# Kernel tuning notes

Hardware: AMD Instinct MI355X
Metric: run time of the kernel (lower is better)

The kernel has to match this reference:

```python
import jax, jax.numpy as jnp
import numpy as np

N = 50000       # num_nodes
R = 8           # num_relations
H = 64          # hidden_channels
C = 16          # num_classes
E = 1_600_000   # num edges (avg degree 32)
T = 8192        # number of 'author' target nodes (first T nodes after to_homogeneous)


def setup_inputs() -> dict:
    key = jax.random.key(0)
    ks = jax.random.split(key, 12)
    s = 0.02
    return {
        "edge_index": jax.random.randint(ks[0], (2, E), 0, N),
        "edge_type": jax.random.randint(ks[1], (E,), 0, R),
        "num_target": T,
        # conv1 (featureless: weight is an embedding table [R, N, H], root is [N, H])
        "weight1": jax.random.normal(ks[2], (R, N, H), jnp.float32) * s,
        "root1": jax.random.normal(ks[3], (N, H), jnp.float32) * s,
        "bias1": jnp.zeros((H,), jnp.float32),
        # conv2
        "weight2": jax.random.normal(ks[4], (R, H, H), jnp.float32) * s,
        "root2": jax.random.normal(ks[5], (H, H), jnp.float32) * s,
        "bias2": jnp.zeros((H,), jnp.float32),
        # linear head
        "lin_w": jax.random.normal(ks[6], (H, C), jnp.float32) * s,
        "lin_b": jnp.zeros((C,), jnp.float32),
    }


def reference(edge_index, edge_type, num_target, weight1, root1, bias1,
              weight2, root2, bias2, lin_w, lin_b):
    src, dst = edge_index[0], edge_index[1]
    E_ = src.shape[0]

    # PyG RGCNConv aggregates with MEAN per relation, then sums over relations.
    # Count edges per (dst node, relation) to form the per-relation mean denominator.
    seg = dst * R + edge_type                          # [E] combined (node, relation) id
    cnt = jax.ops.segment_sum(jnp.ones((E_,), jnp.float32), seg, num_segments=N * R)
    scale = (1.0 / jnp.maximum(cnt, 1.0))[seg]         # [E]

    # ---- conv1: x is None -> message = weight1[edge_type][src] (embedding lookup) ----
    m1 = weight1[edge_type, src] * scale[:, None]      # [E, H]
    h1 = jax.ops.segment_sum(m1, dst, num_segments=N)  # [N, H]
    h1 = h1 + root1 + bias1                            # root1[arange(N)] == root1
    h1 = jax.nn.elu(h1)

    # ---- conv2: message = h1[src] @ weight2[edge_type] ----
    # Precompute per-relation node transforms [R, N, H], then gather per edge.
    hr = jnp.einsum('nh,rhk->rnk', h1, weight2)        # [R, N, H]
    m2 = hr[edge_type, src] * scale[:, None]           # [E, H]
    h2 = jax.ops.segment_sum(m2, dst, num_segments=N)  # [N, H]
    h2 = h2 + h1 @ root2 + bias2
    h2 = jax.nn.elu(h2)

    # ---- linear head on the target ('author') node slice ----
    out = h2[:num_target] @ lin_w + lin_b              # [T, C]
    return out
```

## Files before the change

### kernel.cpp

```cpp
#include <hip/hip_runtime.h>

#define NNODES 50000
#define NREL   8
#define HID    64
#define NCLS   16
#define NEDGE  1600000
#define NTGT   8192
#define NBINS  (NNODES * NREL)
#define CHUNK  1024
#define NCHUNK ((NBINS + CHUNK - 1) / CHUNK)
#define C1PART 12500

__device__ __forceinline__ float elu1(float x) { return x > 0.f ? x : expm1f(x); }

__device__ __forceinline__ int pack_rec(int src, int rel, int cnt) {
  return src | (rel << 16) | (cnt << 19);
}

__global__ void count_kernel(const int* __restrict__ ei, const int* __restrict__ et,
                             int* __restrict__ cnt, int* __restrict__ epos) {
  int e4 = (blockIdx.x * blockDim.x + threadIdx.x) * 4;
  if (e4 >= NEDGE) return;
  int4 d = *(const int4*)(ei + NEDGE + e4);
  int4 r = *(const int4*)(et + e4);
  int4 p;
  p.x = atomicAdd(&cnt[d.x * NREL + r.x], 1);
  p.y = atomicAdd(&cnt[d.y * NREL + r.y], 1);
  p.z = atomicAdd(&cnt[d.z * NREL + r.z], 1);
  p.w = atomicAdd(&cnt[d.w * NREL + r.w], 1);
  *(int4*)(epos + e4) = p;
}

__global__ void chunk_sum_kernel(const int* __restrict__ cnt, int* __restrict__ csum) {
  __shared__ int sw[4];
  int t = threadIdx.x, lane = t & 63, wid = t >> 6;
  int i = blockIdx.x * CHUNK + t * 4;
  int s = 0;
  if (i < NBINS) { int4 c = *(const int4*)(cnt + i); s = c.x + c.y + c.z + c.w; }
#pragma unroll
  for (int off = 32; off >= 1; off >>= 1) s += __shfl_xor(s, off);
  if (lane == 0) sw[wid] = s;
  __syncthreads();
  if (t == 0) csum[blockIdx.x] = sw[0] + sw[1] + sw[2] + sw[3];
}

__global__ void scan_csum_kernel(const int* __restrict__ csum, int* __restrict__ cbase) {
  __shared__ int sw[8];
  int t = threadIdx.x, lane = t & 63, wid = t >> 6;
  int v0 = (t < NCHUNK) ? csum[t] : 0;
  int v = v0;
#pragma unroll
  for (int off = 1; off < 64; off <<= 1) {
    int u = __shfl_up(v, off);
    if (lane >= off) v += u;
  }
  if (lane == 63) sw[wid] = v;
  __syncthreads();
  if (t == 0) {
    int run = 0;
#pragma unroll
    for (int j = 0; j < 8; ++j) { int x = sw[j]; sw[j] = run; run += x; }
  }
  __syncthreads();
  if (t < NCHUNK) cbase[t] = sw[wid] + (v - v0);
}

__global__ void scan_write_kernel(const int* __restrict__ cnt, const int* __restrict__ cbase,
                                  int* __restrict__ binptr) {
  __shared__ int sw[4];
  int t = threadIdx.x, lane = t & 63, wid = t >> 6;
  int i = blockIdx.x * CHUNK + t * 4;
  int4 c = make_int4(0, 0, 0, 0);
  if (i < NBINS) c = *(const int4*)(cnt + i);
  int p0 = c.x, p1 = p0 + c.y, p2 = p1 + c.z, s = p2 + c.w;
  int v = s;
#pragma unroll
  for (int off = 1; off < 64; off <<= 1) {
    int u = __shfl_up(v, off);
    if (lane >= off) v += u;
  }
  if (lane == 63) sw[wid] = v;
  __syncthreads();
  if (t == 0) {
    int run = 0;
#pragma unroll
    for (int j = 0; j < 4; ++j) { int x = sw[j]; sw[j] = run; run += x; }
  }
  __syncthreads();
  if (i < NBINS) {
    int excl = cbase[blockIdx.x] + sw[wid] + (v - s);
    *(int4*)(binptr + i) = make_int4(excl, excl + p0, excl + p1, excl + p2);
  }
  if (blockIdx.x == 0 && t == 0) binptr[NBINS] = NEDGE;
}

__global__ void scatter_kernel(const int* __restrict__ ei, const int* __restrict__ et,
                               const int* __restrict__ epos, const int* __restrict__ binptr,
                               int* __restrict__ epo) {
  int e4 = (blockIdx.x * blockDim.x + threadIdx.x) * 4;
  if (e4 >= NEDGE) return;
  int4 sv = *(const int4*)(ei + e4);
  int4 dv = *(const int4*)(ei + NEDGE + e4);
  int4 rv = *(const int4*)(et + e4);
  int4 pv = *(const int4*)(epos + e4);
  int srcs[4] = {sv.x, sv.y, sv.z, sv.w};
  int dsts[4] = {dv.x, dv.y, dv.z, dv.w};
  int rels[4] = {rv.x, rv.y, rv.z, rv.w};
  int poss[4] = {pv.x, pv.y, pv.z, pv.w};
#pragma unroll
  for (int j = 0; j < 4; ++j) {
    int bin = dsts[j] * NREL + rels[j];
    int b = binptr[bin];
    int c = binptr[bin + 1] - b;
    epo[b + poss[j]] = pack_rec(srcs[j], rels[j], c);
  }
}

__global__ __launch_bounds__(256) void conv1_kernel(
    const int* __restrict__ binptr, const int* __restrict__ epo,
    const float* __restrict__ w1, const float* __restrict__ root1,
    const float* __restrict__ bias1, float* __restrict__ h1, int nodeOff) {
  int wave = nodeOff + blockIdx.x * 4 + (threadIdx.x >> 6);
  if (wave >= NNODES) return;
  int lane = threadIdx.x & 63;
  int g = lane >> 4;
  int col = (lane & 15) << 2;
  int b0 = binptr[wave * NREL], b8 = binptr[wave * NREL + NREL];
  float4 acc = make_float4(0.f, 0.f, 0.f, 0.f);
  for (int eb = b0; eb < b8; eb += 64) {
    int mb = min(64, b8 - eb);
    int q = epo[eb + min(lane, mb - 1)];
    for (int j = 0; j < mb; j += 32) {
      float4 a[8]; float sc[8];
#pragma unroll
      for (int u = 0; u < 8; ++u) {
        int e0 = j + u * 4;
        if (e0 < mb) {
          int ei = e0 + g;
          int eic = min(ei, mb - 1);
          int rec = __shfl(q, eic);
          int src = rec & 0xFFFF;
          int rel = (rec >> 16) & 7;
          int cnt = ((unsigned)rec) >> 19;
          float s = 1.0f / (float)cnt;
          sc[u] = (ei < mb) ? s : 0.f;
          a[u] = *(const float4*)(w1 + (((size_t)(unsigned)(rel * NNODES + src)) << 6) + col);
        } else {
          sc[u] = 0.f;
          a[u] = make_float4(0.f, 0.f, 0.f, 0.f);
        }
      }
#pragma unroll
      for (int u = 0; u < 8; ++u) {
        acc.x = fmaf(a[u].x, sc[u], acc.x);
        acc.y = fmaf(a[u].y, sc[u], acc.y);
        acc.z = fmaf(a[u].z, sc[u], acc.z);
        acc.w = fmaf(a[u].w, sc[u], acc.w);
      }
    }
  }
#pragma unroll
  for (int off = 16; off < 64; off <<= 1) {
    acc.x += __shfl_xor(acc.x, off);
    acc.y += __shfl_xor(acc.y, off);
    acc.z += __shfl_xor(acc.z, off);
    acc.w += __shfl_xor(acc.w, off);
  }
  if (g == 0) {
    const float* rp = root1 + (((size_t)wave) << 6) + col;
    float4 r = *(const float4*)rp;
    float4 bz = *(const float4*)(bias1 + col);
    float4 v;
    v.x = elu1(acc.x + r.x + bz.x);
    v.y = elu1(acc.y + r.y + bz.y);
    v.z = elu1(acc.z + r.z + bz.z);
    v.w = elu1(acc.w + r.w + bz.w);
    *(float4*)(h1 + (((size_t)wave) << 6) + col) = v;
  }
}

__global__ __launch_bounds__(256) void conv2a_kernel(
    const int* __restrict__ binptr, const int* __restrict__ epo,
    const float* __restrict__ h1, float* __restrict__ agg, int nodeBase, int nloc) {
  int wv = blockIdx.x * 4 + (threadIdx.x >> 6);
  if (wv >= nloc * NREL) return;
  int lane = threadIdx.x & 63;
  int g = lane >> 4;
  int col = (lane & 15) << 2;
  int r = wv & 7;
  int bin = (nodeBase + (wv >> 3)) * NREL + r;
  int bb = binptr[bin], ee = binptr[bin + 1];
  float4 s = make_float4(0.f, 0.f, 0.f, 0.f);
  for (int e = bb; e < ee; e += 64) {
    int mb = min(64, ee - e);
    int q = epo[e + min(lane, mb - 1)];
    for (int j = 0; j < mb; j += 16) {
      float4 a[4]; float vld[4];
#pragma unroll
      for (int u = 0; u < 4; ++u) {
        int e0 = j + u * 4;
        if (e0 < mb) {
          int ei = e0 + g;
          int eic = min(ei, mb - 1);
          int src = __shfl(q, eic) & 0xFFFF;
          vld[u] = (ei < mb) ? 1.f : 0.f;
          a[u] = *(const float4*)(h1 + (((size_t)(unsigned)src) << 6) + col);
        } else {
          vld[u] = 0.f;
          a[u] = make_float4(0.f, 0.f, 0.f, 0.f);
        }
      }
#pragma unroll
      for (int u = 0; u < 4; ++u) {
        s.x = fmaf(a[u].x, vld[u], s.x);
        s.y = fmaf(a[u].y, vld[u], s.y);
        s.z = fmaf(a[u].z, vld[u], s.z);
        s.w = fmaf(a[u].w, vld[u], s.w);
      }
    }
  }
#pragma unroll
  for (int off = 16; off < 64; off <<= 1) {
    s.x += __shfl_xor(s.x, off);
    s.y += __shfl_xor(s.y, off);
    s.z += __shfl_xor(s.z, off);
    s.w += __shfl_xor(s.w, off);
  }
  if (g == 0) {
    float scl = (ee > bb) ? 1.0f / (float)(ee - bb) : 0.f;
    float4 o = make_float4(s.x * scl, s.y * scl, s.z * scl, s.w * scl);
    *(float4*)(agg + (((size_t)wv) << 6) + col) = o;
  }
}

__global__ __launch_bounds__(256, 4) void conv2b_kernel(
    const float* __restrict__ agg, const float* __restrict__ h1,
    const float* __restrict__ w2, const float* __restrict__ root2,
    const float* __restrict__ bias2, const float* __restrict__ lin_w,
    const float* __restrict__ lin_b, float* __restrict__ out, int nodeBase) {
  __shared__ float sW[HID * HID];
  int t = threadIdx.x, lane = t & 63, wid = t >> 6;
  int ln0 = blockIdx.x * 8 + wid * 2;
  float bz = bias2[lane];
  float o0 = bz, o1 = bz;
  for (int r = 0; r < NREL; ++r) {
    if (r) __syncthreads();
#pragma unroll
    for (int i = 0; i < 4; ++i)
      *(float4*)(sW + t * 4 + i * 1024) = *(const float4*)(w2 + (r << 12) + t * 4 + i * 1024);
    __syncthreads();
    const float* a0 = agg + (((size_t)((ln0 + 0) * NREL + r)) << 6);
    const float* a1 = agg + (((size_t)((ln0 + 1) * NREL + r)) << 6);
#pragma unroll 16
    for (int k = 0; k < HID; ++k) {
      float w = sW[(k << 6) + lane];
      o0 = fmaf(a0[k], w, o0);
      o1 = fmaf(a1[k], w, o1);
    }
  }
  __syncthreads();
#pragma unroll
  for (int i = 0; i < 4; ++i)
    *(float4*)(sW + t * 4 + i * 1024) = *(const float4*)(root2 + t * 4 + i * 1024);
  __syncthreads();
  int g0 = nodeBase + ln0;
  const float* r0p = h1 + ((size_t)(g0 + 0) << 6);
  const float* r1p = h1 + ((size_t)(g0 + 1) << 6);
#pragma unroll 16
  for (int k = 0; k < HID; ++k) {
    float w = sW[(k << 6) + lane];
    o0 = fmaf(r0p[k], w, o0);
    o1 = fmaf(r1p[k], w, o1);
  }
  __syncthreads();
  int row0 = wid * 2;
  sW[row0 * 65 + lane] = elu1(o0);
  sW[(row0 + 1) * 65 + lane] = elu1(o1);
  float* lw = sW + 8 * 65;
  *(float4*)(lw + t * 4) = *(const float4*)(lin_w + t * 4);
  __syncthreads();
  if (t < 8 * NCLS) {
    int n = t >> 4, c = t & 15;
    float accv = lin_b[c];
#pragma unroll 16
    for (int l = 0; l < HID; ++l)
      accv = fmaf(sW[n * 65 + l], lw[l * NCLS + c], accv);
    out[((size_t)(nodeBase + blockIdx.x * 8 + n)) * NCLS + c] = accv;
  }
}

extern "C" void kernel_launch(void* const* d_in, const int* in_sizes, int n_in,
                              void* d_out, int out_size, void* d_ws, size_t ws_size,
                              hipStream_t stream) {
  const int*   ei    = (const int*)d_in[0];
  const int*   et    = (const int*)d_in[1];
  const float* w1    = (const float*)d_in[3];
  const float* root1 = (const float*)d_in[4];
  const float* bias1 = (const float*)d_in[5];
  const float* w2    = (const float*)d_in[6];
  const float* root2 = (const float*)d_in[7];
  const float* bias2 = (const float*)d_in[8];
  const float* lin_w = (const float*)d_in[9];
  const float* lin_b = (const float*)d_in[10];
  float* out = (float*)d_out;

  char* ws = (char*)d_ws;
  float* h1     = (float*)ws;
  int*   cnt    = (int*)ws;
  int*   epos   = (int*)(ws + (size_t)NBINS * 4);
  char*  p      = ws + (size_t)NNODES * HID * 4;
  int*   binptr = (int*)p;  p += ((size_t)(NBINS + 1) * 4 + 255) & ~(size_t)255;
  int*   csum   = (int*)p;  p += ((size_t)NCHUNK * 4 + 255) & ~(size_t)255;
  int*   cbase  = (int*)p;  p += ((size_t)NCHUNK * 4 + 255) & ~(size_t)255;
  int*   epo    = (int*)p;  p += (size_t)NEDGE * 4;
  float* agg    = (float*)p;
  size_t fixed  = (size_t)(p - ws);
  int chunk = (fixed + (size_t)NTGT * NREL * HID * 4 <= ws_size) ? NTGT : NTGT / 2;

  hipMemsetAsync(cnt, 0, (size_t)NBINS * sizeof(int), stream);
  count_kernel<<<(NEDGE / 4 + 255) / 256, 256, 0, stream>>>(ei, et, cnt, epos);
  chunk_sum_kernel<<<NCHUNK, 256, 0, stream>>>(cnt, csum);
  scan_csum_kernel<<<1, 512, 0, stream>>>(csum, cbase);
  scan_write_kernel<<<NCHUNK, 256, 0, stream>>>(cnt, cbase, binptr);
  scatter_kernel<<<(NEDGE / 4 + 255) / 256, 256, 0, stream>>>(ei, et, epos, binptr, epo);
  for (int s4 = 0; s4 < 4; ++s4)
    conv1_kernel<<<C1PART / 4, 256, 0, stream>>>(binptr, epo, w1, root1, bias1, h1,
                                                 s4 * C1PART);
  for (int c = 0; c < NTGT / chunk; ++c) {
    conv2a_kernel<<<(chunk * NREL) / 4, 256, 0, stream>>>(binptr, epo, h1, agg, c * chunk, chunk);
    conv2b_kernel<<<chunk / 8, 256, 0, stream>>>(agg, h1, w2, root2, bias2, lin_w, lin_b,
                                                 out, c * chunk);
  }
}
```

Before: 420.4 us.

## Pad per-bin counters to 64-byte stride and launch conv1 as one kernel

```diff
diff --git a/kernel.cpp b/kernel.cpp
--- a/kernel.cpp
+++ b/kernel.cpp
@@ -9,7 +9,6 @@
 #define NBINS  (NNODES * NREL)
 #define CHUNK  1024
 #define NCHUNK ((NBINS + CHUNK - 1) / CHUNK)
-#define C1PART 12500
 
 __device__ __forceinline__ float elu1(float x) { return x > 0.f ? x : expm1f(x); }
 
@@ -24,10 +23,10 @@
   int4 d = *(const int4*)(ei + NEDGE + e4);
   int4 r = *(const int4*)(et + e4);
   int4 p;
-  p.x = atomicAdd(&cnt[d.x * NREL + r.x], 1);
-  p.y = atomicAdd(&cnt[d.y * NREL + r.y], 1);
-  p.z = atomicAdd(&cnt[d.z * NREL + r.z], 1);
-  p.w = atomicAdd(&cnt[d.w * NREL + r.w], 1);
+  p.x = atomicAdd(&cnt[(d.x * NREL + r.x) << 4], 1);
+  p.y = atomicAdd(&cnt[(d.y * NREL + r.y) << 4], 1);
+  p.z = atomicAdd(&cnt[(d.z * NREL + r.z) << 4], 1);
+  p.w = atomicAdd(&cnt[(d.w * NREL + r.w) << 4], 1);
   *(int4*)(epos + e4) = p;
 }
 
@@ -36,7 +35,9 @@
   int t = threadIdx.x, lane = t & 63, wid = t >> 6;
   int i = blockIdx.x * CHUNK + t * 4;
   int s = 0;
-  if (i < NBINS) { int4 c = *(const int4*)(cnt + i); s = c.x + c.y + c.z + c.w; }
+  if (i < NBINS)
+    s = cnt[(size_t)(i + 0) << 4] + cnt[(size_t)(i + 1) << 4] +
+        cnt[(size_t)(i + 2) << 4] + cnt[(size_t)(i + 3) << 4];
 #pragma unroll
   for (int off = 32; off >= 1; off >>= 1) s += __shfl_xor(s, off);
   if (lane == 0) sw[wid] = s;
@@ -70,9 +71,14 @@
   __shared__ int sw[4];
   int t = threadIdx.x, lane = t & 63, wid = t >> 6;
   int i = blockIdx.x * CHUNK + t * 4;
-  int4 c = make_int4(0, 0, 0, 0);
-  if (i < NBINS) c = *(const int4*)(cnt + i);
-  int p0 = c.x, p1 = p0 + c.y, p2 = p1 + c.z, s = p2 + c.w;
+  int c0 = 0, c1 = 0, c2 = 0, c3 = 0;
+  if (i < NBINS) {
+    c0 = cnt[(size_t)(i + 0) << 4];
+    c1 = cnt[(size_t)(i + 1) << 4];
+    c2 = cnt[(size_t)(i + 2) << 4];
+    c3 = cnt[(size_t)(i + 3) << 4];
+  }
+  int p0 = c0, p1 = p0 + c1, p2 = p1 + c2, s = p2 + c3;
   int v = s;
 #pragma unroll
   for (int off = 1; off < 64; off <<= 1) {
@@ -119,8 +125,8 @@
 __global__ __launch_bounds__(256) void conv1_kernel(
     const int* __restrict__ binptr, const int* __restrict__ epo,
     const float* __restrict__ w1, const float* __restrict__ root1,
-    const float* __restrict__ bias1, float* __restrict__ h1, int nodeOff) {
-  int wave = nodeOff + blockIdx.x * 4 + (threadIdx.x >> 6);
+    const float* __restrict__ bias1, float* __restrict__ h1) {
+  int wave = blockIdx.x * 4 + (threadIdx.x >> 6);
   if (wave >= NNODES) return;
   int lane = threadIdx.x & 63;
   int g = lane >> 4;
@@ -305,27 +311,28 @@
   float* out = (float*)d_out;
 
   char* ws = (char*)d_ws;
-  float* h1     = (float*)ws;
-  int*   cnt    = (int*)ws;
-  int*   epos   = (int*)(ws + (size_t)NBINS * 4);
-  char*  p      = ws + (size_t)NNODES * HID * 4;
+  int*   epos   = (int*)ws;
+  char*  p      = ws + (size_t)NEDGE * 4;
   int*   binptr = (int*)p;  p += ((size_t)(NBINS + 1) * 4 + 255) & ~(size_t)255;
   int*   csum   = (int*)p;  p += ((size_t)NCHUNK * 4 + 255) & ~(size_t)255;
   int*   cbase  = (int*)p;  p += ((size_t)NCHUNK * 4 + 255) & ~(size_t)255;
-  int*   epo    = (int*)p;  p += (size_t)NEDGE * 4;
-  float* agg    = (float*)p;
-  size_t fixed  = (size_t)(p - ws);
-  int chunk = (fixed + (size_t)NTGT * NREL * HID * 4 <= ws_size) ? NTGT : NTGT / 2;
-
-  hipMemsetAsync(cnt, 0, (size_t)NBINS * sizeof(int), stream);
+  int*   cnt    = (int*)p;
+  float* h1     = (float*)p;
+  char*  q      = p + (size_t)NNODES * HID * 4;
+  int*   epo    = (int*)q;  q += (size_t)NEDGE * 4;
+  float* agg    = (float*)q;
+  size_t cnt_end = (size_t)((p + (size_t)NBINS * 64) - ws);
+  size_t agg_end = (size_t)(q - ws) + (size_t)NTGT * NREL * HID * 4;
+  size_t need8k  = (agg_end > cnt_end) ? agg_end : cnt_end;
+  int chunk = (need8k <= ws_size) ? NTGT : NTGT / 2;
+
+  hipMemsetAsync(cnt, 0, (size_t)NBINS * 64, stream);
   count_kernel<<<(NEDGE / 4 + 255) / 256, 256, 0, stream>>>(ei, et, cnt, epos);
   chunk_sum_kernel<<<NCHUNK, 256, 0, stream>>>(cnt, csum);
   scan_csum_kernel<<<1, 512, 0, stream>>>(csum, cbase);
   scan_write_kernel<<<NCHUNK, 256, 0, stream>>>(cnt, cbase, binptr);
   scatter_kernel<<<(NEDGE / 4 + 255) / 256, 256, 0, stream>>>(ei, et, epos, binptr, epo);
-  for (int s4 = 0; s4 < 4; ++s4)
-    conv1_kernel<<<C1PART / 4, 256, 0, stream>>>(binptr, epo, w1, root1, bias1, h1,
-                                                 s4 * C1PART);
+  conv1_kernel<<<(NNODES + 3) / 4, 256, 0, stream>>>(binptr, epo, w1, root1, bias1, h1);
   for (int c = 0; c < NTGT / chunk; ++c) {
     conv2a_kernel<<<(chunk * NREL) / 4, 256, 0, stream>>>(binptr, epo, h1, agg, c * chunk, chunk);
     conv2b_kernel<<<chunk / 8, 256, 0, stream>>>(agg, h1, w2, root2, bias2, lin_w, lin_b,
```

Result: faster. 410.3 us (-2.4%).

## Replace three-pass scan with single-pass decoupled look-back scan and merge launches

Applied to the files above, without the earlier changes.

```diff
diff --git a/kernel.cpp b/kernel.cpp
--- a/kernel.cpp
+++ b/kernel.cpp
@@ -6,10 +6,10 @@
 #define NCLS   16
 #define NEDGE  1600000
 #define NTGT   8192
+#define HALF   4096
 #define NBINS  (NNODES * NREL)
 #define CHUNK  1024
 #define NCHUNK ((NBINS + CHUNK - 1) / CHUNK)
-#define C1PART 12500
 
 __device__ __forceinline__ float elu1(float x) { return x > 0.f ? x : expm1f(x); }
 
@@ -17,9 +17,19 @@
   return src | (rel << 16) | (cnt << 19);
 }
 
+__device__ __forceinline__ unsigned long long ld_stat(unsigned long long* p) {
+  return __hip_atomic_load(p, __ATOMIC_RELAXED, __HIP_MEMORY_SCOPE_AGENT);
+}
+__device__ __forceinline__ void st_stat(unsigned long long* p, unsigned long long v) {
+  __hip_atomic_store(p, v, __ATOMIC_RELAXED, __HIP_MEMORY_SCOPE_AGENT);
+}
+
 __global__ void count_kernel(const int* __restrict__ ei, const int* __restrict__ et,
-                             int* __restrict__ cnt, int* __restrict__ epos) {
-  int e4 = (blockIdx.x * blockDim.x + threadIdx.x) * 4;
+                             int* __restrict__ cnt, int* __restrict__ epos,
+                             unsigned long long* __restrict__ status) {
+  int gt = blockIdx.x * blockDim.x + threadIdx.x;
+  if (gt < NCHUNK) status[gt] = 0;
+  int e4 = gt * 4;
   if (e4 >= NEDGE) return;
   int4 d = *(const int4*)(ei + NEDGE + e4);
   int4 r = *(const int4*)(et + e4);
@@ -31,24 +41,19 @@
   *(int4*)(epos + e4) = p;
 }
 
-__global__ void chunk_sum_kernel(const int* __restrict__ cnt, int* __restrict__ csum) {
+__global__ __launch_bounds__(256) void scan_lb_kernel(
+    const int* __restrict__ cnt, unsigned long long* __restrict__ status,
+    int* __restrict__ binptr) {
   __shared__ int sw[4];
+  __shared__ int srun;
+  __shared__ int sbase;
   int t = threadIdx.x, lane = t & 63, wid = t >> 6;
-  int i = blockIdx.x * CHUNK + t * 4;
-  int s = 0;
-  if (i < NBINS) { int4 c = *(const int4*)(cnt + i); s = c.x + c.y + c.z + c.w; }
-#pragma unroll
-  for (int off = 32; off >= 1; off >>= 1) s += __shfl_xor(s, off);
-  if (lane == 0) sw[wid] = s;
-  __syncthreads();
-  if (t == 0) csum[blockIdx.x] = sw[0] + sw[1] + sw[2] + sw[3];
-}
-
-__global__ void scan_csum_kernel(const int* __restrict__ csum, int* __restrict__ cbase) {
-  __shared__ int sw[8];
-  int t = threadIdx.x, lane = t & 63, wid = t >> 6;
-  int v0 = (t < NCHUNK) ? csum[t] : 0;
-  int v = v0;
+  int c = blockIdx.x;
+  int i = c * CHUNK + t * 4;
+  int4 cv = make_int4(0, 0, 0, 0);
+  if (i < NBINS) cv = *(const int4*)(cnt + i);
+  int p0 = cv.x, p1 = p0 + cv.y, p2 = p1 + cv.z, s = p2 + cv.w;
+  int v = s;
 #pragma unroll
   for (int off = 1; off < 64; off <<= 1) {
     int u = __shfl_up(v, off);
@@ -59,39 +64,56 @@
   if (t == 0) {
     int run = 0;
 #pragma unroll
-    for (int j = 0; j < 8; ++j) { int x = sw[j]; sw[j] = run; run += x; }
-  }
-  __syncthreads();
-  if (t < NCHUNK) cbase[t] = sw[wid] + (v - v0);
-}
-
-__global__ void scan_write_kernel(const int* __restrict__ cnt, const int* __restrict__ cbase,
-                                  int* __restrict__ binptr) {
-  __shared__ int sw[4];
-  int t = threadIdx.x, lane = t & 63, wid = t >> 6;
-  int i = blockIdx.x * CHUNK + t * 4;
-  int4 c = make_int4(0, 0, 0, 0);
-  if (i < NBINS) c = *(const int4*)(cnt + i);
-  int p0 = c.x, p1 = p0 + c.y, p2 = p1 + c.z, s = p2 + c.w;
-  int v = s;
-#pragma unroll
-  for (int off = 1; off < 64; off <<= 1) {
-    int u = __shfl_up(v, off);
-    if (lane >= off) v += u;
-  }
-  if (lane == 63) sw[wid] = v;
-  __syncthreads();
-  if (t == 0) {
-    int run = 0;
-#pragma unroll
     for (int j = 0; j < 4; ++j) { int x = sw[j]; sw[j] = run; run += x; }
-  }
-  __syncthreads();
+    srun = run;
+    unsigned long long f = (c == 0) ? 2ull : 1ull;
+    st_stat(&status[c], (f << 62) | (unsigned)run);
+    if (c == 0) sbase = 0;
+  }
+  __syncthreads();
+  if (c > 0 && t < 64) {
+    long long tot = 0;
+    int back = c - 1;
+    for (;;) {
+      int idx = back - lane;
+      unsigned long long st = (2ull << 62);
+      if (idx >= 0) st = ld_stat(&status[idx]);
+      int flag = (int)(st >> 62);
+      bool isinc = (idx < 0) || (flag == 2);
+      bool isval = (idx < 0) || (flag >= 1);
+      unsigned long long incb = __ballot(isinc);
+      unsigned long long valb = __ballot(isval);
+      unsigned long long notval = ~valb;
+      int firstinv = notval ? (__ffsll((long long)notval) - 1) : 64;
+      int firstinc = incb ? (__ffsll((long long)incb) - 1) : 64;
+      if (firstinc < firstinv) {
+        int val = (lane <= firstinc) ? (int)(st & 0xFFFFFFFFu) : 0;
+#pragma unroll
+        for (int off = 32; off >= 1; off >>= 1) val += __shfl_xor(val, off);
+        tot += val;
+        break;
+      } else if (firstinv > 0) {
+        int val = (lane < firstinv) ? (int)(st & 0xFFFFFFFFu) : 0;
+#pragma unroll
+        for (int off = 32; off >= 1; off >>= 1) val += __shfl_xor(val, off);
+        tot += val;
+        back -= firstinv;
+      } else {
+        __builtin_amdgcn_s_sleep(2);
+      }
+    }
+    if (lane == 0) {
+      sbase = (int)tot;
+      st_stat(&status[c], (2ull << 62) | (unsigned)((int)tot + srun));
+    }
+  }
+  __syncthreads();
+  int base = sbase;
   if (i < NBINS) {
-    int excl = cbase[blockIdx.x] + sw[wid] + (v - s);
+    int excl = base + sw[wid] + (v - s);
     *(int4*)(binptr + i) = make_int4(excl, excl + p0, excl + p1, excl + p2);
   }
-  if (blockIdx.x == 0 && t == 0) binptr[NBINS] = NEDGE;
+  if (c == 0 && t == 0) binptr[NBINS] = NEDGE;
 }
 
 __global__ void scatter_kernel(const int* __restrict__ ei, const int* __restrict__ et,
@@ -119,8 +141,8 @@
 __global__ __launch_bounds__(256) void conv1_kernel(
     const int* __restrict__ binptr, const int* __restrict__ epo,
     const float* __restrict__ w1, const float* __restrict__ root1,
-    const float* __restrict__ bias1, float* __restrict__ h1, int nodeOff) {
-  int wave = nodeOff + blockIdx.x * 4 + (threadIdx.x >> 6);
+    const float* __restrict__ bias1, float* __restrict__ h1) {
+  int wave = blockIdx.x * 4 + (threadIdx.x >> 6);
   if (wave >= NNODES) return;
   int lane = threadIdx.x & 63;
   int g = lane >> 4;
@@ -167,8 +189,7 @@
     acc.w += __shfl_xor(acc.w, off);
   }
   if (g == 0) {
-    const float* rp = root1 + (((size_t)wave) << 6) + col;
-    float4 r = *(const float4*)rp;
+    float4 r = *(const float4*)(root1 + (((size_t)wave) << 6) + col);
     float4 bz = *(const float4*)(bias1 + col);
     float4 v;
     v.x = elu1(acc.x + r.x + bz.x);
@@ -228,8 +249,8 @@
   }
   if (g == 0) {
     float scl = (ee > bb) ? 1.0f / (float)(ee - bb) : 0.f;
-    float4 o = make_float4(s.x * scl, s.y * scl, s.z * scl, s.w * scl);
-    *(float4*)(agg + (((size_t)wv) << 6) + col) = o;
+    *(float4*)(agg + (((size_t)wv) << 6) + col) =
+        make_float4(s.x * scl, s.y * scl, s.z * scl, s.w * scl);
   }
 }
 
@@ -310,25 +331,19 @@
   int*   epos   = (int*)(ws + (size_t)NBINS * 4);
   char*  p      = ws + (size_t)NNODES * HID * 4;
   int*   binptr = (int*)p;  p += ((size_t)(NBINS + 1) * 4 + 255) & ~(size_t)255;
-  int*   csum   = (int*)p;  p += ((size_t)NCHUNK * 4 + 255) & ~(size_t)255;
-  int*   cbase  = (int*)p;  p += ((size_t)NCHUNK * 4 + 255) & ~(size_t)255;
+  unsigned long long* status = (unsigned long long*)p;
+  p += ((size_t)NCHUNK * 8 + 255) & ~(size_t)255;
   int*   epo    = (int*)p;  p += (size_t)NEDGE * 4;
   float* agg    = (float*)p;
-  size_t fixed  = (size_t)(p - ws);
-  int chunk = (fixed + (size_t)NTGT * NREL * HID * 4 <= ws_size) ? NTGT : NTGT / 2;
 
   hipMemsetAsync(cnt, 0, (size_t)NBINS * sizeof(int), stream);
-  count_kernel<<<(NEDGE / 4 + 255) / 256, 256, 0, stream>>>(ei, et, cnt, epos);
-  chunk_sum_kernel<<<NCHUNK, 256, 0, stream>>>(cnt, csum);
-  scan_csum_kernel<<<1, 512, 0, stream>>>(csum, cbase);
-  scan_write_kernel<<<NCHUNK, 256, 0, stream>>>(cnt, cbase, binptr);
+  count_kernel<<<(NEDGE / 4 + 255) / 256, 256, 0, stream>>>(ei, et, cnt, epos, status);
+  scan_lb_kernel<<<NCHUNK, 256, 0, stream>>>(cnt, status, binptr);
   scatter_kernel<<<(NEDGE / 4 + 255) / 256, 256, 0, stream>>>(ei, et, epos, binptr, epo);
-  for (int s4 = 0; s4 < 4; ++s4)
-    conv1_kernel<<<C1PART / 4, 256, 0, stream>>>(binptr, epo, w1, root1, bias1, h1,
-                                                 s4 * C1PART);
-  for (int c = 0; c < NTGT / chunk; ++c) {
-    conv2a_kernel<<<(chunk * NREL) / 4, 256, 0, stream>>>(binptr, epo, h1, agg, c * chunk, chunk);
-    conv2b_kernel<<<chunk / 8, 256, 0, stream>>>(agg, h1, w2, root2, bias2, lin_w, lin_b,
-                                                 out, c * chunk);
-  }
-}
+  conv1_kernel<<<(NNODES + 3) / 4, 256, 0, stream>>>(binptr, epo, w1, root1, bias1, h1);
+  for (int c = 0; c < 2; ++c) {
+    conv2a_kernel<<<(HALF * NREL) / 4, 256, 0, stream>>>(binptr, epo, h1, agg, c * HALF, HALF);
+    conv2b_kernel<<<HALF / 8, 256, 0, stream>>>(agg, h1, w2, root2, bias2, lin_w, lin_b,
+                                                out, c * HALF);
+  }
+}
```

Result: faster. 406.9 us (-3.2%).
